# Performance work log

Hardware: AMD Instinct MI355X
Metric: run time of the kernel (lower is better)

## Reference

```python
import jax, jax.numpy as jnp
import numpy as np

B, S, D = 16, 2048, 128
SCALE = 1.0 / float(np.sqrt(D))  # scale = 1/sqrt(dim_K) per docstring


def setup_inputs() -> dict:
    key = jax.random.key(0)
    kq, kk, kv = jax.random.split(key, 3)
    Q = jax.random.normal(kq, (B, S, D), dtype=jnp.float32)
    K = jax.random.normal(kk, (B, S, D), dtype=jnp.float32)
    V = jax.random.normal(kv, (B, S, D), dtype=jnp.float32)
    return {"Q": Q, "K": K, "V": V}


def reference(Q, K, V):
    # attention = Q @ K^T * scale  -> [B, S, S]
    attn = jnp.einsum('bqd,bkd->bqk', Q, K) * SCALE
    attn = jax.nn.softmax(attn, axis=-1)
    # context = attn @ V -> [B, S, D]
    context = jnp.einsum('bqk,bkd->bqd', attn, V)
    return context
```

## Files before the change

kernel.cpp:

```cpp
#include <hip/hip_runtime.h>
#include <hip/hip_bf16.h>


#define NB 16
#define NS 2048
#define ND 128
#define KVB 32
#define NTT (NS / KVB)
#define IMG 16384
#define QSC (0.08838834764831845f * 1.4426950408889634f)

typedef __attribute__((ext_vector_type(8))) short bf16x8;
typedef __attribute__((ext_vector_type(4))) short short4v;
typedef __attribute__((ext_vector_type(16))) float f32x16;
typedef __attribute__((ext_vector_type(4))) int int4v;

__device__ __forceinline__ short f2bf(float f) {
    unsigned u = __builtin_bit_cast(unsigned, f);
    return (short)((u + 0x7fffu + ((u >> 16) & 1u)) >> 16);
}

#if __has_builtin(__builtin_amdgcn_exp2f)
#define EXP2F(x) __builtin_amdgcn_exp2f(x)
#else
#define EXP2F(x) __expf((x) * 0.6931471805599453f)
#endif

__device__ __forceinline__ void gll16(const void* g, void* l) {
    __builtin_amdgcn_global_load_lds(
        (const __attribute__((address_space(1))) uint32_t*)g,
        (__attribute__((address_space(3))) uint32_t*)l, 16, 0, 0);
}

__global__ __launch_bounds__(256, 2)
void prep_kv(const float* __restrict__ Kg, const float* __restrict__ Vg,
             uint8_t* __restrict__ ws) {
    __shared__ __align__(16) uint8_t img[2 * IMG];
    const int tid = threadIdx.x;
    const int t = blockIdx.x, b = blockIdx.y;
    const float* Kb = Kg + ((size_t)b * NS + (size_t)t * 64) * ND;
    const float* Vb = Vg + ((size_t)b * NS + (size_t)t * 64) * ND;
#pragma unroll
    for (int it = 0; it < 8; ++it) {
        int idx = it * 256 + tid;
        int r  = idx >> 5;
        int c4 = (idx & 31) << 2;
        int sub = (r >> 5) * (2 * 8192);
        int rr = r & 31;
        float4 kvv = *(const float4*)(Kb + (size_t)r * ND + c4);
        short4v ks = { f2bf(kvv.x), f2bf(kvv.y), f2bf(kvv.z), f2bf(kvv.w) };
        *(short4v*)&img[sub + rr * 256 + ((c4 * 2) ^ ((rr & 7) << 4))] = ks;
        float4 vv = *(const float4*)(Vb + (size_t)r * ND + c4);
        float vf[4] = { vv.x, vv.y, vv.z, vv.w };
#pragma unroll
        for (int di = 0; di < 4; ++di) {
            int d = c4 + di;
            *(short*)&img[sub + 8192 + d * 64 + ((rr * 2) ^ (((d >> 1) & 3) << 4))]
                = f2bf(vf[di]);
        }
    }
    __syncthreads();
    float4* dst = (float4*)(ws + (size_t)(b * (NTT / 2) + t) * (2 * IMG));
    const float4* srcl = (const float4*)img;
#pragma unroll
    for (int j = 0; j < 8; ++j)
        dst[j * 256 + tid] = srcl[j * 256 + tid];
}

__global__ __launch_bounds__(768, 3)
void sdpa_fwd(const float* __restrict__ Qg, const uint8_t* __restrict__ ws,
              float* __restrict__ Og) {
    __shared__ __align__(16) uint8_t kv[2][3][IMG];

    const int tid  = threadIdx.x;
    const int w    = tid >> 6;
    const int wq   = w & 3;
    const int wh   = w >> 2;
    const int lane = tid & 63;
    const int lr_  = lane & 31;
    const int hi   = lane >> 5;

    const int tlo  = (wh == 0) ? 0 : (22 + 21 * (wh - 1));
    const int tcnt = (wh == 0) ? 22 : 21;

    const int gid  = blockIdx.x;
    const int b    = (gid & 7) * 2 + ((gid >> 3) & 1);
    const int qblk = gid >> 4;
    const int q0w  = qblk * 128 + wq * 32;

    bf16x8 qf[8];
    {
        const float* qrow = Qg + ((size_t)b * NS + q0w + lr_) * ND;
#pragma unroll
        for (int dc = 0; dc < 8; ++dc) {
            const float4* p = (const float4*)(qrow + dc * 16 + hi * 8);
            float4 x0 = p[0], x1 = p[1];
            bf16x8 f;
            f[0] = f2bf(x0.x * QSC); f[1] = f2bf(x0.y * QSC);
            f[2] = f2bf(x0.z * QSC); f[3] = f2bf(x0.w * QSC);
            f[4] = f2bf(x1.x * QSC); f[5] = f2bf(x1.y * QSC);
            f[6] = f2bf(x1.z * QSC); f[7] = f2bf(x1.w * QSC);
            qf[dc] = f;
        }
    }

    f32x16 acc[4];
#pragma unroll
    for (int n = 0; n < 4; ++n)
#pragma unroll
        for (int r = 0; r < 16; ++r) acc[n][r] = 0.f;
    float l_run = 0.f;

    const uint8_t* wsb = ws + (size_t)b * NTT * IMG;

    auto stage = [&](int bfi, int it) {
        if (it < tcnt) {
            const uint8_t* src = wsb + (size_t)(tlo + it) * IMG
                                     + (size_t)(wq * 4096 + lane * 16);
            uint8_t* dst = &kv[bfi][wh][wq * 4096];
#pragma unroll
            for (int i = 0; i < 4; ++i)
                gll16(src + i * 1024, dst + i * 1024);
        }
    };

    const int kbase = lr_ * 256 + ((hi * 16) ^ ((lr_ & 7) << 4));
    const int vbase = 8192 + lr_ * 64 + ((hi * 16) ^ (((lr_ >> 1) & 3) << 4));

    int buf = 0;
    stage(0, 0);
    __syncthreads();

    for (int t = 0; t < 22; ++t) {
        stage(buf ^ 1, t + 1);

        if (t < tcnt) {
            const uint8_t* img = kv[buf][wh];

            f32x16 sa, sb;
#pragma unroll
            for (int r = 0; r < 16; ++r) { sa[r] = 0.f; sb[r] = 0.f; }
            __builtin_amdgcn_s_setprio(1);
#pragma unroll
            for (int dc = 0; dc < 4; ++dc) {
                bf16x8 k0 = *(const bf16x8*)(img + (kbase ^ ((2 * dc) * 32)));
                bf16x8 k1 = *(const bf16x8*)(img + (kbase ^ ((2 * dc + 1) * 32)));
                sa = __builtin_amdgcn_mfma_f32_32x32x16_bf16(k0, qf[2*dc],   sa, 0, 0, 0);
                sb = __builtin_amdgcn_mfma_f32_32x32x16_bf16(k1, qf[2*dc+1], sb, 0, 0, 0);
            }
            __builtin_amdgcn_s_setprio(0);

            f32x16 s0 = sa + sb;
#pragma unroll
            for (int r = 0; r < 16; ++r) s0[r] = EXP2F(s0[r]);
            {
                float u0 = (s0[0] + s0[1])   + (s0[2] + s0[3]);
                float u1 = (s0[4] + s0[5])   + (s0[6] + s0[7]);
                float u2 = (s0[8] + s0[9])   + (s0[10] + s0[11]);
                float u3 = (s0[12] + s0[13]) + (s0[14] + s0[15]);
                l_run += (u0 + u1) + (u2 + u3);
            }

            int W[8];
#define PK(dst, x, y) asm("v_cvt_pk_bf16_f32 %0, %1, %2" : "=v"(dst) : "v"(x), "v"(y))
            PK(W[0], s0[0],  s0[1]);  PK(W[1], s0[2],  s0[3]);
            PK(W[2], s0[4],  s0[5]);  PK(W[3], s0[6],  s0[7]);
            PK(W[4], s0[8],  s0[9]);  PK(W[5], s0[10], s0[11]);
            PK(W[6], s0[12], s0[13]); PK(W[7], s0[14], s0[15]);
#undef PK
            bf16x8 pa[2];
#pragma unroll
            for (int g = 0; g < 2; ++g) {
                int a0 = W[g * 4 + 0], b0 = W[g * 4 + 2];
                int a1 = W[g * 4 + 1], b1 = W[g * 4 + 3];
                asm("v_permlane32_swap_b32 %0, %1" : "+v"(a0), "+v"(b0));
                asm("v_permlane32_swap_b32 %0, %1" : "+v"(a1), "+v"(b1));
                int4v A = { a0, a1, b0, b1 };
                pa[g] = __builtin_bit_cast(bf16x8, A);
            }

            __builtin_amdgcn_s_setprio(1);
#pragma unroll
            for (int n = 0; n < 4; ++n) {
#pragma unroll
                for (int kc = 0; kc < 2; ++kc) {
                    bf16x8 vf = *(const bf16x8*)(img + ((vbase ^ (kc * 32)) + n * 2048));
                    acc[n] = __builtin_amdgcn_mfma_f32_32x32x16_bf16(pa[kc], vf, acc[n], 0, 0, 0);
                }
            }
            __builtin_amdgcn_s_setprio(0);
        }

        __syncthreads();
        buf ^= 1;
    }

    l_run += __shfl_xor(l_run, 32);

    float* scr = (float*)&kv[0][0][0];
    const int sbase = wq * 4224 + lane * 66;
#pragma unroll
    for (int rnd = 1; rnd <= 2; ++rnd) {
        __syncthreads();
        if (wh == rnd) {
#pragma unroll
            for (int n = 0; n < 4; ++n)
#pragma unroll
                for (int r = 0; r < 16; ++r) scr[sbase + n * 16 + r] = acc[n][r];
            scr[sbase + 64] = l_run;
        }
        __syncthreads();
        if (wh == 0) {
            l_run += scr[sbase + 64];
#pragma unroll
            for (int n = 0; n < 4; ++n)
#pragma unroll
                for (int r = 0; r < 16; ++r)
                    acc[n][r] += scr[sbase + n * 16 + r];
        }
    }

    if (wh == 0) {
        float* ob = Og + ((size_t)b * NS + q0w) * ND + lr_;
#pragma unroll
        for (int r = 0; r < 16; ++r) {
            int row = (r & 3) + 8 * (r >> 2) + 4 * hi;
            float li = 1.f / __shfl(l_run, row);
#pragma unroll
            for (int n = 0; n < 4; ++n)
                ob[(size_t)row * ND + n * 32] = acc[n][r] * li;
        }
    }
}

extern "C" void kernel_launch(void* const* d_in, const int* in_sizes, int n_in,
                              void* d_out, int out_size, void* d_ws, size_t ws_size,
                              hipStream_t stream) {
    const float* Q = (const float*)d_in[0];
    const float* K = (const float*)d_in[1];
    const float* V = (const float*)d_in[2];
    float* O = (float*)d_out;
    (void)in_sizes; (void)n_in; (void)out_size; (void)ws_size;
    uint8_t* ws = (uint8_t*)d_ws;
    prep_kv<<<dim3(NS / 64, NB), 256, 0, stream>>>(K, V, ws);
    sdpa_fwd<<<dim3(NB * NS / 128, 1), 768, 0, stream>>>(Q, ws, O);
}
```

Before: 59.57 us.

## Split KV across two wave groups with four-buffer staging and paired tiles

The block shrinks from 12 waves that split the KV sequence three ways to 8 waves that split it in half. Each half now stages two KV tiles ahead into a four-slot LDS ring. It processes two tiles per barrier, issuing both QK^T products before both softmax/PV steps to add instruction-level parallelism and halve the number of block syncs. The cross-group reduction collapses to a single scratch exchange fused into the output write. In exchange there are fewer resident waves to hide latency, and LDS use grows to 128KB per block.

```diff
diff --git a/kernel.cpp b/kernel.cpp
--- a/kernel.cpp
+++ b/kernel.cpp
@@ -7,6 +7,7 @@
 #define ND 128
 #define KVB 32
 #define NTT (NS / KVB)
+#define NHT (NTT / 2)
 #define IMG 16384
 #define QSC (0.08838834764831845f * 1.4426950408889634f)
 
@@ -67,10 +68,10 @@
         dst[j * 256 + tid] = srcl[j * 256 + tid];
 }
 
-__global__ __launch_bounds__(768, 3)
+__global__ __launch_bounds__(512, 2)
 void sdpa_fwd(const float* __restrict__ Qg, const uint8_t* __restrict__ ws,
               float* __restrict__ Og) {
-    __shared__ __align__(16) uint8_t kv[2][3][IMG];
+    __shared__ __align__(16) uint8_t kv[2][4][IMG];
 
     const int tid  = threadIdx.x;
     const int w    = tid >> 6;
@@ -80,8 +81,7 @@
     const int lr_  = lane & 31;
     const int hi   = lane >> 5;
 
-    const int tlo  = (wh == 0) ? 0 : (22 + 21 * (wh - 1));
-    const int tcnt = (wh == 0) ? 22 : 21;
+    const int tlo  = wh * NHT;
 
     const int gid  = blockIdx.x;
     const int b    = (gid & 7) * 2 + ((gid >> 3) & 1);
@@ -113,11 +113,11 @@
 
     const uint8_t* wsb = ws + (size_t)b * NTT * IMG;
 
-    auto stage = [&](int bfi, int it) {
-        if (it < tcnt) {
-            const uint8_t* src = wsb + (size_t)(tlo + it) * IMG
+    auto stage = [&](int bufidx, int t) {
+        if (t < NHT) {
+            const uint8_t* src = wsb + (size_t)(tlo + t) * IMG
                                      + (size_t)(wq * 4096 + lane * 16);
-            uint8_t* dst = &kv[bfi][wh][wq * 4096];
+            uint8_t* dst = &kv[wh][bufidx][wq * 4096];
 #pragma unroll
             for (int i = 0; i < 4; ++i)
                 gll16(src + i * 1024, dst + i * 1024);
@@ -127,108 +127,115 @@
     const int kbase = lr_ * 256 + ((hi * 16) ^ ((lr_ & 7) << 4));
     const int vbase = 8192 + lr_ * 64 + ((hi * 16) ^ (((lr_ >> 1) & 3) << 4));
 
-    int buf = 0;
+    auto qk2 = [&](const uint8_t* img, f32x16& s) {
+        f32x16 sa, sb;
+#pragma unroll
+        for (int r = 0; r < 16; ++r) { sa[r] = 0.f; sb[r] = 0.f; }
+        __builtin_amdgcn_s_setprio(1);
+#pragma unroll
+        for (int dc = 0; dc < 4; ++dc) {
+            bf16x8 k0 = *(const bf16x8*)(img + (kbase ^ ((2 * dc) * 32)));
+            bf16x8 k1 = *(const bf16x8*)(img + (kbase ^ ((2 * dc + 1) * 32)));
+            sa = __builtin_amdgcn_mfma_f32_32x32x16_bf16(k0, qf[2*dc],   sa, 0, 0, 0);
+            sb = __builtin_amdgcn_mfma_f32_32x32x16_bf16(k1, qf[2*dc+1], sb, 0, 0, 0);
+        }
+        __builtin_amdgcn_s_setprio(0);
+        s = sa + sb;
+    };
+
+    auto smpv = [&](f32x16& s0, const uint8_t* img) {
+#pragma unroll
+        for (int r = 0; r < 16; ++r) s0[r] = EXP2F(s0[r]);
+        {
+            float u0 = (s0[0] + s0[1])   + (s0[2] + s0[3]);
+            float u1 = (s0[4] + s0[5])   + (s0[6] + s0[7]);
+            float u2 = (s0[8] + s0[9])   + (s0[10] + s0[11]);
+            float u3 = (s0[12] + s0[13]) + (s0[14] + s0[15]);
+            l_run += (u0 + u1) + (u2 + u3);
+        }
+        int W[8];
+#define PK(dst, x, y) asm("v_cvt_pk_bf16_f32 %0, %1, %2" : "=v"(dst) : "v"(x), "v"(y))
+        PK(W[0], s0[0],  s0[1]);  PK(W[1], s0[2],  s0[3]);
+        PK(W[2], s0[4],  s0[5]);  PK(W[3], s0[6],  s0[7]);
+        PK(W[4], s0[8],  s0[9]);  PK(W[5], s0[10], s0[11]);
+        PK(W[6], s0[12], s0[13]); PK(W[7], s0[14], s0[15]);
+#undef PK
+        bf16x8 pa[2];
+#pragma unroll
+        for (int g = 0; g < 2; ++g) {
+            int a0 = W[g * 4 + 0], b0 = W[g * 4 + 2];
+            int a1 = W[g * 4 + 1], b1 = W[g * 4 + 3];
+            asm("v_permlane32_swap_b32 %0, %1" : "+v"(a0), "+v"(b0));
+            asm("v_permlane32_swap_b32 %0, %1" : "+v"(a1), "+v"(b1));
+            int4v A = { a0, a1, b0, b1 };
+            pa[g] = __builtin_bit_cast(bf16x8, A);
+        }
+        __builtin_amdgcn_s_setprio(1);
+#pragma unroll
+        for (int n = 0; n < 4; ++n) {
+#pragma unroll
+            for (int kc = 0; kc < 2; ++kc) {
+                bf16x8 vf = *(const bf16x8*)(img + ((vbase ^ (kc * 32)) + n * 2048));
+                acc[n] = __builtin_amdgcn_mfma_f32_32x32x16_bf16(pa[kc], vf, acc[n], 0, 0, 0);
+            }
+        }
+        __builtin_amdgcn_s_setprio(0);
+    };
+
+    const uint8_t* b0_ = &kv[wh][0][0];
+    const uint8_t* b1_ = &kv[wh][1][0];
+    const uint8_t* b2_ = &kv[wh][2][0];
+    const uint8_t* b3_ = &kv[wh][3][0];
+
     stage(0, 0);
+    stage(1, 1);
     __syncthreads();
 
-    for (int t = 0; t < 22; ++t) {
-        stage(buf ^ 1, t + 1);
-
-        if (t < tcnt) {
-            const uint8_t* img = kv[buf][wh];
-
-            f32x16 sa, sb;
-#pragma unroll
-            for (int r = 0; r < 16; ++r) { sa[r] = 0.f; sb[r] = 0.f; }
-            __builtin_amdgcn_s_setprio(1);
-#pragma unroll
-            for (int dc = 0; dc < 4; ++dc) {
-                bf16x8 k0 = *(const bf16x8*)(img + (kbase ^ ((2 * dc) * 32)));
-                bf16x8 k1 = *(const bf16x8*)(img + (kbase ^ ((2 * dc + 1) * 32)));
-                sa = __builtin_amdgcn_mfma_f32_32x32x16_bf16(k0, qf[2*dc],   sa, 0, 0, 0);
-                sb = __builtin_amdgcn_mfma_f32_32x32x16_bf16(k1, qf[2*dc+1], sb, 0, 0, 0);
-            }
-            __builtin_amdgcn_s_setprio(0);
-
-            f32x16 s0 = sa + sb;
-#pragma unroll
-            for (int r = 0; r < 16; ++r) s0[r] = EXP2F(s0[r]);
-            {
-                float u0 = (s0[0] + s0[1])   + (s0[2] + s0[3]);
-                float u1 = (s0[4] + s0[5])   + (s0[6] + s0[7]);
-                float u2 = (s0[8] + s0[9])   + (s0[10] + s0[11]);
-                float u3 = (s0[12] + s0[13]) + (s0[14] + s0[15]);
-                l_run += (u0 + u1) + (u2 + u3);
-            }
-
-            int W[8];
-#define PK(dst, x, y) asm("v_cvt_pk_bf16_f32 %0, %1, %2" : "=v"(dst) : "v"(x), "v"(y))
-            PK(W[0], s0[0],  s0[1]);  PK(W[1], s0[2],  s0[3]);
-            PK(W[2], s0[4],  s0[5]);  PK(W[3], s0[6],  s0[7]);
-            PK(W[4], s0[8],  s0[9]);  PK(W[5], s0[10], s0[11]);
-            PK(W[6], s0[12], s0[13]); PK(W[7], s0[14], s0[15]);
-#undef PK
-            bf16x8 pa[2];
-#pragma unroll
-            for (int g = 0; g < 2; ++g) {
-                int a0 = W[g * 4 + 0], b0 = W[g * 4 + 2];
-                int a1 = W[g * 4 + 1], b1 = W[g * 4 + 3];
-                asm("v_permlane32_swap_b32 %0, %1" : "+v"(a0), "+v"(b0));
-                asm("v_permlane32_swap_b32 %0, %1" : "+v"(a1), "+v"(b1));
-                int4v A = { a0, a1, b0, b1 };
-                pa[g] = __builtin_bit_cast(bf16x8, A);
-            }
-
-            __builtin_amdgcn_s_setprio(1);
-#pragma unroll
-            for (int n = 0; n < 4; ++n) {
-#pragma unroll
-                for (int kc = 0; kc < 2; ++kc) {
-                    bf16x8 vf = *(const bf16x8*)(img + ((vbase ^ (kc * 32)) + n * 2048));
-                    acc[n] = __builtin_amdgcn_mfma_f32_32x32x16_bf16(pa[kc], vf, acc[n], 0, 0, 0);
-                }
-            }
-            __builtin_amdgcn_s_setprio(0);
-        }
-
+    f32x16 sA, sB;
+    for (int i2 = 0; i2 < 8; ++i2) {
+        const int base = i2 * 4;
+        stage(2, base + 2);
+        stage(3, base + 3);
+        qk2(b0_, sA);
+        qk2(b1_, sB);
+        smpv(sA, b0_);
+        smpv(sB, b1_);
         __syncthreads();
-        buf ^= 1;
+        stage(0, base + 4);
+        stage(1, base + 5);
+        qk2(b2_, sA);
+        qk2(b3_, sB);
+        smpv(sA, b2_);
+        smpv(sB, b3_);
+        __syncthreads();
     }
 
     l_run += __shfl_xor(l_run, 32);
 
     float* scr = (float*)&kv[0][0][0];
     const int sbase = wq * 4224 + lane * 66;
-#pragma unroll
-    for (int rnd = 1; rnd <= 2; ++rnd) {
-        __syncthreads();
-        if (wh == rnd) {
-#pragma unroll
-            for (int n = 0; n < 4; ++n)
-#pragma unroll
-                for (int r = 0; r < 16; ++r) scr[sbase + n * 16 + r] = acc[n][r];
-            scr[sbase + 64] = l_run;
-        }
-        __syncthreads();
-        if (wh == 0) {
-            l_run += scr[sbase + 64];
-#pragma unroll
-            for (int n = 0; n < 4; ++n)
-#pragma unroll
-                for (int r = 0; r < 16; ++r)
-                    acc[n][r] += scr[sbase + n * 16 + r];
-        }
-    }
-
+    if (wh == 1) {
+#pragma unroll
+        for (int n = 0; n < 4; ++n)
+#pragma unroll
+            for (int r = 0; r < 16; ++r) scr[sbase + n * 16 + r] = acc[n][r];
+        scr[sbase + 64] = l_run;
+    }
+    __syncthreads();
     if (wh == 0) {
+        float lc = l_run + scr[sbase + 64];
+        float li[16];
+#pragma unroll
+        for (int r = 0; r < 16; ++r)
+            li[r] = 1.f / __shfl(lc, (r & 3) + 8 * (r >> 2) + 4 * hi);
         float* ob = Og + ((size_t)b * NS + q0w) * ND + lr_;
 #pragma unroll
         for (int r = 0; r < 16; ++r) {
             int row = (r & 3) + 8 * (r >> 2) + 4 * hi;
-            float li = 1.f / __shfl(l_run, row);
 #pragma unroll
             for (int n = 0; n < 4; ++n)
-                ob[(size_t)row * ND + n * 32] = acc[n][r] * li;
+                ob[(size_t)row * ND + n * 32] =
+                    (acc[n][r] + scr[sbase + n * 16 + r]) * li[r];
         }
     }
 }
@@ -243,5 +250,5 @@
     (void)in_sizes; (void)n_in; (void)out_size; (void)ws_size;
     uint8_t* ws = (uint8_t*)d_ws;
     prep_kv<<<dim3(NS / 64, NB), 256, 0, stream>>>(K, V, ws);
-    sdpa_fwd<<<dim3(NB * NS / 128, 1), 768, 0, stream>>>(Q, ws, O);
-}
+    sdpa_fwd<<<dim3(NB * NS / 128, 1), 512, 0, stream>>>(Q, ws, O);
+}
```

Result: faster. 57.93 us (-2.8%).
